# Kernel optimization log

Measured on AMD Instinct MI355X. Metric: run time of the kernel, lower is better.

The kernel has to match this reference:

```python
import math
import jax, jax.numpy as jnp
import numpy as np

NUM_HEADS = 16


def setup_inputs() -> dict:
    key = jax.random.key(0)
    ks = jax.random.split(key, 5)
    B, S, H = 2, 2048, 1024
    hidden_states = jax.random.normal(ks[0], (B, S, H), dtype=jnp.float32)
    # causal lower-triangular float mask [1, 1, S, S], as the module expects
    ltor_mask = jnp.tril(jnp.ones((S, S), dtype=jnp.float32))[None, None, :, :]
    # weights stored pre-transposed: y = x @ W + b (equivalent to torch Linear)
    W_qkv = jax.random.normal(ks[1], (H, 3 * H), dtype=jnp.float32) * (1.0 / math.sqrt(H))
    b_qkv = jnp.zeros((3 * H,), dtype=jnp.float32)
    W_dense = jax.random.normal(ks[2], (H, H), dtype=jnp.float32) * (1.0 / math.sqrt(H))
    b_dense = jnp.zeros((H,), dtype=jnp.float32)
    return {
        "hidden_states": hidden_states,
        "ltor_mask": ltor_mask,
        "W_qkv": W_qkv,
        "b_qkv": b_qkv,
        "W_dense": W_dense,
        "b_dense": b_dense,
    }


def reference(hidden_states, ltor_mask, W_qkv, b_qkv, W_dense, b_dense):
    B, S, H = hidden_states.shape
    nh = NUM_HEADS
    hd = H // nh

    # fused QKV projection: [B, S, 3H] -> split -> [B, nh, S, hd]
    qkv = hidden_states @ W_qkv + b_qkv
    q, k, v = jnp.split(qkv, 3, axis=-1)

    def to_heads(x):
        return x.reshape(B, S, nh, hd).transpose(0, 2, 1, 3)

    q, k, v = to_heads(q), to_heads(k), to_heads(v)

    # scaled dot-product scores [B, nh, S, S]
    scores = jnp.einsum("bhqd,bhkd->bhqk", q, k) / math.sqrt(hd)
    # mul/sub causal masking, exactly as the torch module does
    scores = scores * ltor_mask - 10000.0 * (1.0 - ltor_mask)
    probs = jax.nn.softmax(scores, axis=-1)
    # attention dropout omitted (eval mode / p=0.0)

    ctx = jnp.einsum("bhqk,bhkd->bhqd", probs, v)
    ctx = ctx.transpose(0, 2, 1, 3).reshape(B, S, H)

    out = ctx @ W_dense + b_dense
    # output dropout omitted (eval mode / p=0.0)
    return out
```

## Files before the change

### kernel.cpp

```cpp
#include <hip/hip_runtime.h>
#include <math.h>

#define BATCH 2
#define SEQ   2048
#define HID   1024
#define NHEAD 16
#define HDIM  64
#define MTOT  (BATCH * SEQ)
#define QKVN  (3 * HID)
#define HBUF  ((size_t)BATCH * NHEAD * SEQ * HDIM)

typedef _Float16 f16x8 __attribute__((ext_vector_type(8)));
typedef _Float16 f16x4 __attribute__((ext_vector_type(4)));
typedef float    f32x4 __attribute__((ext_vector_type(4)));

#define MFMA16(a, b, c) __builtin_amdgcn_mfma_f32_16x16x32_f16((a), (b), (c), 0, 0, 0)

#define GLDS16(gp, lp) __builtin_amdgcn_global_load_lds( \
    (const __attribute__((address_space(1))) void*)(gp), \
    (__attribute__((address_space(3))) void*)(lp), 16, 0, 0)

#if __has_builtin(__builtin_amdgcn_exp2f)
#define EXP2F(x) __builtin_amdgcn_exp2f(x)
#else
#define EXP2F(x) exp2f(x)
#endif

#define SCALE2 0.18033688011f
#define MASK2  -14426.950408f
#define BIAS2  -4.0f

__global__ __launch_bounds__(256) void prep_kernel(
    const float* __restrict__ hs, const float* __restrict__ Wqkv,
    const float* __restrict__ Wd, _Float16* __restrict__ A_h,
    _Float16* __restrict__ outQ, _Float16* __restrict__ outD)
{
    __shared__ _Float16 T[32][36];
    const int gid = blockIdx.x;
    const int tid = threadIdx.x;
    if (gid < 2048) {
        const int ci = gid * 256 + tid;
        const int m = ci >> 7, cc = ci & 127;
        const float* src = hs + (size_t)m * 1024 + cc * 8;
        f16x8 o;
#pragma unroll
        for (int j = 0; j < 8; ++j) o[j] = (_Float16)src[j];
        *(f16x8*)(A_h + (size_t)m * 1024 + ((cc >> 3) << 6)
                  + (((cc & 7) ^ (m & 7)) << 3)) = o;
        return;
    }
    const int tb = gid - 2048;
    const int bx = tb & 127, k0 = (tb >> 7) * 32;
    const float* in;
    _Float16* out;
    int N, n0;
    bool isQ;
    if (bx < 96) { in = Wqkv; out = outQ; N = QKVN; n0 = bx * 32; isQ = true; }
    else         { in = Wd;   out = outD; N = HID;  n0 = (bx - 96) * 32; isQ = false; }
    {
        const int r = tid >> 3, c4 = (tid & 7) * 4;
        float4 v = *(const float4*)(in + (size_t)(k0 + r) * N + n0 + c4);
        T[r][c4 + 0] = (_Float16)v.x;
        T[r][c4 + 1] = (_Float16)v.y;
        T[r][c4 + 2] = (_Float16)v.z;
        T[r][c4 + 3] = (_Float16)v.w;
    }
    __syncthreads();
    {
        const int nn = tid >> 3, k4 = (tid & 7) * 4;
        const int n = n0 + nn;
        f16x4 o;
        o[0] = T[k4 + 0][nn]; o[1] = T[k4 + 1][nn];
        o[2] = T[k4 + 2][nn]; o[3] = T[k4 + 3][nn];
        if (isQ) {
            const int cin = (((k0 >> 5) & 1) << 2) | (k4 >> 3);
            const int pos = cin ^ (n & 7);
            *(f16x4*)(out + (size_t)n * 1024 + (k0 & ~63) + pos * 8 + (k4 & 7)) = o;
        } else {
            const int pos = ((k4 >> 3) ^ (n & 3)), half = (k4 >> 2) & 1;
            *(f16x4*)(out + (size_t)n * 1024 + k0 + pos * 8 + half * 4) = o;
        }
    }
}

__global__ __launch_bounds__(512, 2) void qkv_gemm8(
    const _Float16* __restrict__ A, const _Float16* __restrict__ Bt,
    const float* __restrict__ bias, _Float16* __restrict__ base)
{
    __shared__ _Float16 S[2][2][16384];
    const int tid = threadIdx.x;
    const int w = tid >> 6, l = tid & 63;
    const int a = l & 15, q4 = l >> 4, a7 = a & 7;
    const int xc = blockIdx.x & 7, loc = blockIdx.x >> 3;
    const int bx = (xc & 1) * 6 + loc % 6;
    const int by = (xc >> 1) * 4 + loc / 6;
    const int m0 = by * 256, n0 = bx * 256;
    const int wm = (w >> 2) * 128, wn = (w & 3) * 64;

    const int srow = tid >> 3;
    const int scol = (tid & 7) * 8;
    const _Float16* gAs = A  + (size_t)(m0 + srow) * 1024 + scol;
    const _Float16* gBs = Bt + (size_t)(n0 + srow) * 1024 + scol;

    auto stage_u = [&](int u, int kt, int sl) {
        const size_t ko = (size_t)kt * 64;
        if (u < 4)
            GLDS16(gAs + (size_t)u * 65536 + ko, &S[sl][0][0] + u * 4096 + tid * 8);
        else
            GLDS16(gBs + (size_t)(u - 4) * 65536 + ko, &S[sl][1][0] + (u - 4) * 4096 + tid * 8);
    };

#pragma unroll
    for (int u = 0; u < 8; ++u) stage_u(u, 0, 0);
#pragma unroll
    for (int u = 0; u < 8; ++u) stage_u(u, 1, 1);
    asm volatile("s_waitcnt vmcnt(8)" ::: "memory");
    __builtin_amdgcn_sched_barrier(0);
    __builtin_amdgcn_s_barrier();
    __builtin_amdgcn_sched_barrier(0);

    f32x4 acc[8][4];
#pragma unroll
    for (int i = 0; i < 8; ++i)
#pragma unroll
        for (int j = 0; j < 4; ++j) acc[i][j] = (f32x4){0.f, 0.f, 0.f, 0.f};

#define FRG(SP, row_, ks_) \
    (*(const f16x8*)&(SP)[(row_) * 64 + ((((ks_) * 4 + q4) ^ a7) << 3)])

    f16x8 afL[4][2], afH[4][2], bfL[2][2], bfH[2][2];
    {
        const _Float16* sA = &S[0][0][0];
        const _Float16* sB = &S[0][1][0];
#pragma unroll
        for (int i = 0; i < 4; ++i) {
            afL[i][0] = FRG(sA, wm + i * 16 + a, 0);
            afL[i][1] = FRG(sA, wm + i * 16 + a, 1);
        }
#pragma unroll
        for (int j = 0; j < 2; ++j) {
            bfL[j][0] = FRG(sB, wn + j * 16 + a, 0);
            bfL[j][1] = FRG(sB, wn + j * 16 + a, 1);
        }
    }

    for (int t = 0; t < 16; ++t) {
        const int sl = t & 1, nsl = sl ^ 1;
        const _Float16* sA = &S[sl][0][0];
        const _Float16* sB = &S[sl][1][0];
        const bool st = (t >= 1) & (t < 15);

        if (st) {
#pragma unroll
            for (int u = 0; u < 8; ++u) stage_u(u, t + 1, nsl);
        }

        __builtin_amdgcn_s_setprio(1);
#pragma unroll
        for (int i = 0; i < 4; ++i)
#pragma unroll
            for (int j = 0; j < 2; ++j) {
                acc[i][j] = MFMA16(afL[i][0], bfL[j][0], acc[i][j]);
                acc[i][j] = MFMA16(afL[i][1], bfL[j][1], acc[i][j]);
            }
        __builtin_amdgcn_s_setprio(0);

#pragma unroll
        for (int j = 0; j < 2; ++j) {
            bfH[j][0] = FRG(sB, wn + 32 + j * 16 + a, 0);
            bfH[j][1] = FRG(sB, wn + 32 + j * 16 + a, 1);
        }
        __builtin_amdgcn_s_setprio(1);
#pragma unroll
        for (int i = 0; i < 4; ++i)
#pragma unroll
            for (int j = 0; j < 2; ++j) {
                acc[i][j + 2] = MFMA16(afL[i][0], bfH[j][0], acc[i][j + 2]);
                acc[i][j + 2] = MFMA16(afL[i][1], bfH[j][1], acc[i][j + 2]);
            }
        __builtin_amdgcn_s_setprio(0);

#pragma unroll
        for (int i = 0; i < 4; ++i) {
            afH[i][0] = FRG(sA, wm + 64 + i * 16 + a, 0);
            afH[i][1] = FRG(sA, wm + 64 + i * 16 + a, 1);
        }
        __builtin_amdgcn_s_setprio(1);
#pragma unroll
        for (int i = 0; i < 4; ++i)
#pragma unroll
            for (int j = 0; j < 2; ++j) {
                acc[i + 4][j + 2] = MFMA16(afH[i][0], bfH[j][0], acc[i + 4][j + 2]);
                acc[i + 4][j + 2] = MFMA16(afH[i][1], bfH[j][1], acc[i + 4][j + 2]);
            }
#pragma unroll
        for (int i = 0; i < 4; ++i)
#pragma unroll
            for (int j = 0; j < 2; ++j) {
                acc[i + 4][j] = MFMA16(afH[i][0], bfL[j][0], acc[i + 4][j]);
                acc[i + 4][j] = MFMA16(afH[i][1], bfL[j][1], acc[i + 4][j]);
            }
        __builtin_amdgcn_s_setprio(0);

        asm volatile("s_waitcnt vmcnt(0)" ::: "memory");
        __builtin_amdgcn_sched_barrier(0);
        __builtin_amdgcn_s_barrier();
        __builtin_amdgcn_sched_barrier(0);

        if (t < 15) {
            const _Float16* nA = &S[nsl][0][0];
            const _Float16* nB = &S[nsl][1][0];
#pragma unroll
            for (int i = 0; i < 4; ++i) {
                afL[i][0] = FRG(nA, wm + i * 16 + a, 0);
                afL[i][1] = FRG(nA, wm + i * 16 + a, 1);
            }
#pragma unroll
            for (int j = 0; j < 2; ++j) {
                bfL[j][0] = FRG(nB, wn + j * 16 + a, 0);
                bfL[j][1] = FRG(nB, wn + j * 16 + a, 1);
            }
        }
    }
#undef FRG

#pragma unroll
    for (int j = 0; j < 4; ++j) {
        const int n = n0 + wn + 16 * j + a;
        const float bv = bias[n];
        const int tq = n >> 10, h = (n >> 6) & 15, d = n & 63;
#pragma unroll
        for (int i = 0; i < 8; ++i) {
            const int mb = m0 + wm + 16 * i + q4 * 4;
            const int bb = mb >> 11, sb = mb & 2047;
            if (tq == 2) {
                f16x4 ov;
#pragma unroll
                for (int r = 0; r < 4; ++r) ov[r] = (_Float16)(acc[i][j][r] + bv);
                const size_t off =
                    ((size_t)((bb * 16 + h) * 64 + d)) * 2048
                    + (sb & ~63)
                    + ((((sb >> 3) & 7) ^ (d & 7)) << 3) + (sb & 7);
                *(f16x4*)(base + 3 * HBUF + off) = ov;
            } else if (tq == 1) {
#pragma unroll
                for (int r = 0; r < 4; ++r) {
                    const int s = sb + r;
                    const _Float16 val = (_Float16)(acc[i][j][r] + bv);
                    const int dk = ((((d >> 3) ^ (s & 7)) & 7) << 3) | (d & 7);
                    base[HBUF + ((size_t)(bb * 16 + h) * 2048 + s) * 64 + dk] = val;
                }
            } else {
#pragma unroll
                for (int r = 0; r < 4; ++r) {
                    const _Float16 val = (_Float16)(acc[i][j][r] + bv);
                    base[((size_t)(bb * 16 + h) * 2048 + sb + r) * 64 + d] = val;
                }
            }
        }
    }
}

template<int EPI, int TM>
__global__ __launch_bounds__(256) void mfma_gemm(
    const _Float16* __restrict__ A, const _Float16* __restrict__ Bt,
    const float* __restrict__ bias, void* __restrict__ Cout,
    int M, int N, int K)
{
    __shared__ _Float16 As[TM * 32];
    __shared__ _Float16 Bs[128 * 32];
    constexpr int TI = TM / 32;
    constexpr int AR = TM / 4;

    const int tid = threadIdx.x;
    const int w = tid >> 6, l = tid & 63;
    const int a = l & 15, q4 = l >> 4;
    const int m0 = blockIdx.y * TM, n0 = blockIdx.x * 128;
    const int wm = (w >> 1) * (TM / 2), wn = (w & 1) * 64;

    f32x4 acc[TI][4];
#pragma unroll
    for (int i = 0; i < TI; ++i)
#pragma unroll
        for (int j = 0; j < 4; ++j) acc[i][j] = (f32x4){0.f, 0.f, 0.f, 0.f};

    const _Float16* gA = A + (size_t)(m0 + w * AR + (l >> 2)) * K + (l & 3) * 8;
    const _Float16* gB = Bt + (size_t)(n0 + w * 32 + (l >> 2)) * K + (l & 3) * 8;
    _Float16* sA = As + w * AR * 32;
    _Float16* sB = Bs + w * 1024;

    for (int k0 = 0; k0 < K; k0 += 32) {
#pragma unroll
        for (int u = 0; u < TM / 64; ++u)
            GLDS16(gA + (size_t)u * 16 * K + k0, sA + u * 512);
        GLDS16(gB + k0,          sB);
        GLDS16(gB + 16 * K + k0, sB + 512);
        __syncthreads();

        f16x8 af[TI], bf[4];
        const int pa = (q4 ^ (a & 3)) << 3;
#pragma unroll
        for (int i = 0; i < TI; ++i)
            af[i] = *(const f16x8*)&As[(wm + 16 * i + a) * 32 + pa];
#pragma unroll
        for (int j = 0; j < 4; ++j)
            bf[j] = *(const f16x8*)&Bs[(wn + 16 * j + a) * 32 + pa];
#pragma unroll
        for (int i = 0; i < TI; ++i)
#pragma unroll
            for (int j = 0; j < 4; ++j)
                acc[i][j] = MFMA16(af[i], bf[j], acc[i][j]);
        __syncthreads();
    }

    {
        float* C = (float*)Cout;
#pragma unroll
        for (int j = 0; j < 4; ++j) {
            const int n = n0 + wn + 16 * j + a;
            const float bv = bias[n];
#pragma unroll
            for (int i = 0; i < TI; ++i)
#pragma unroll
                for (int r = 0; r < 4; ++r) {
                    const int m = m0 + wm + 16 * i + q4 * 4 + r;
                    C[(size_t)m * N + n] = acc[i][j][r] + bv;
                }
        }
    }
}

__global__ __launch_bounds__(256, 2) void attn_mfma(
    const _Float16* __restrict__ qb, const _Float16* __restrict__ kb,
    const _Float16* __restrict__ vtb, _Float16* __restrict__ ctx)
{
    __shared__ _Float16 Ks[2][64 * 64];
    __shared__ _Float16 VT[2][64 * 64];
    __shared__ _Float16 Ps[4][16 * 64];

    const int bid = blockIdx.x;
    const int jj = bid >> 3;
    const int bhIdx = (bid & 7) * 4 + (jj >> 4);
    const int p = jj & 15;
    const int b = bhIdx >> 4, h = bhIdx & 15;
    const int tid = threadIdx.x;
    const int w = tid >> 6, l = tid & 63;
    const int a = l & 15, q4 = l >> 4, a7 = a & 7;
    const size_t bh  = ((size_t)b * NHEAD + h) * SEQ;
    const size_t bhd = ((size_t)b * NHEAD + h) * 64;

    const int qHi = (31 - p) * 64 + w * 16;
    const int qLo = p * 64 + w * 16;
    const int ntiles = 32 - p;

    f16x8 qfh[2], qfl[2];
    {
        const _Float16* qp = qb + (bh + qHi + a) * 64;
        qfh[0] = *(const f16x8*)(qp + q4 * 8);
        qfh[1] = *(const f16x8*)(qp + 32 + q4 * 8);
        const _Float16* ql = qb + (bh + qLo + a) * 64;
        qfl[0] = *(const f16x8*)(ql + q4 * 8);
        qfl[1] = *(const f16x8*)(ql + 32 + q4 * 8);
    }

    f32x4 Oh[4], Ol[4];
#pragma unroll
    for (int c = 0; c < 4; ++c) {
        Oh[c] = (f32x4){0.f, 0.f, 0.f, 0.f};
        Ol[c] = (f32x4){0.f, 0.f, 0.f, 0.f};
    }
    float lh = 0.f, ll = 0.f;

    const _Float16* kg = kb + (bh + w * 16) * 64 + l * 8;
    const int vrow = w * 16 + (l >> 3);
    const _Float16* vg = vtb + (bhd + vrow) * 2048 + (l & 7) * 8;
    _Float16* pbuf = &Ps[w][0];
    const int p0 = (q4 ^ a7) << 3;

    auto stage = [&](int t, int buf) {
        _Float16* ksl = &Ks[buf][0] + w * 1024 + l * 8;
        const _Float16* kt = kg + (size_t)t * 4096;
        GLDS16(kt,       ksl);
        GLDS16(kt + 512, ksl + 512);
        _Float16* vtl = &VT[buf][0] + vrow * 64 + (l & 7) * 8;
        GLDS16(vg + t * 64,            vtl);
        GLDS16(vg + t * 64 + 8 * 2048, vtl + 512);
    };

    stage(0, 0);

    for (int t = 0; t < ntiles; ++t) {
        __syncthreads();
        if (t + 1 < ntiles) stage(t + 1, (t + 1) & 1);

        const _Float16* ksb  = &Ks[t & 1][0];
        const _Float16* vbuf = &VT[t & 1][0];
        const int kt0 = t * 64;
        const bool doLo = (t <= p);

        f32x4 sh[4], sl[4];
#pragma unroll
        for (int n0 = 0; n0 < 4; ++n0) {
            f16x8 kf0 = *(const f16x8*)&ksb[(n0 * 16 + a) * 64 + p0];
            f16x8 kf1 = *(const f16x8*)&ksb[(n0 * 16 + a) * 64 + (p0 ^ 32)];
            f32x4 c = (f32x4){0.f, 0.f, 0.f, 0.f};
            c = MFMA16(kf0, qfh[0], c);
            c = MFMA16(kf1, qfh[1], c);
            sh[n0] = c;
            if (doLo) {
                f32x4 d = (f32x4){0.f, 0.f, 0.f, 0.f};
                d = MFMA16(kf0, qfl[0], d);
                d = MFMA16(kf1, qfl[1], d);
                sl[n0] = d;
            }
        }

        auto half_step = [&](f32x4 st[4], float& lrun, f32x4* O,
                             const bool maskT, const int qbase) {
            if (maskT) {
#pragma unroll
                for (int n0 = 0; n0 < 4; ++n0)
#pragma unroll
                    for (int r = 0; r < 4; ++r) {
                        const int kgl = kt0 + n0 * 16 + q4 * 4 + r;
                        st[n0][r] = (kgl > qbase + a) ? MASK2
                                                      : fmaf(st[n0][r], SCALE2, BIAS2);
                    }
            } else {
#pragma unroll
                for (int n0 = 0; n0 < 4; ++n0)
#pragma unroll
                    for (int r = 0; r < 4; ++r)
                        st[n0][r] = fmaf(st[n0][r], SCALE2, BIAS2);
            }
            float ls = 0.f;
#pragma unroll
            for (int n0 = 0; n0 < 4; ++n0)
#pragma unroll
                for (int r = 0; r < 4; ++r) {
                    const float pe = EXP2F(st[n0][r]);
                    st[n0][r] = pe;
                    ls += pe;
                }
            lrun += ls;
#pragma unroll
            for (int n0 = 0; n0 < 4; ++n0) {
                f16x4 pk;
#pragma unroll
                for (int r = 0; r < 4; ++r) pk[r] = (_Float16)st[n0][r];
                const int pos = (2 * n0 + (q4 >> 1)) ^ a7;
                *(f16x4*)&pbuf[a * 64 + pos * 8 + ((q4 & 1) << 2)] = pk;
            }
            f16x8 pf0 = *(const f16x8*)&pbuf[a * 64 + p0];
            f16x8 pf1 = *(const f16x8*)&pbuf[a * 64 + (p0 ^ 32)];
#pragma unroll
            for (int c = 0; c < 4; ++c) {
                f16x8 vf0 = *(const f16x8*)&vbuf[(c * 16 + a) * 64 + p0];
                f16x8 vf1 = *(const f16x8*)&vbuf[(c * 16 + a) * 64 + (p0 ^ 32)];
                O[c] = MFMA16(vf0, pf0, O[c]);
                O[c] = MFMA16(vf1, pf1, O[c]);
            }
        };

        half_step(sh, lh, Oh, t == 31 - p, qHi);
        if (doLo) half_step(sl, ll, Ol, t == p, qLo);
    }

    auto finish = [&](float lrun, const f32x4* O, const int qbase) {
        float lt = lrun;
        lt += __shfl_xor(lt, 16);
        lt += __shfl_xor(lt, 32);
        const float inv = 1.0f / lt;
        const size_t row = (size_t)b * SEQ + qbase + a;
#pragma unroll
        for (int c = 0; c < 4; ++c) {
            const int d0 = c * 16 + q4 * 4;
            const int kcol = h * 64 + (d0 & ~31)
                           + ((((d0 >> 3) & 3) ^ (a & 3)) << 3) + (d0 & 7);
            f16x4 ov;
#pragma unroll
            for (int r = 0; r < 4; ++r) ov[r] = (_Float16)(O[c][r] * inv);
            *(f16x4*)(ctx + row * HID + kcol) = ov;
        }
    };
    finish(lh, Oh, qHi);
    finish(ll, Ol, qLo);
}

extern "C" void kernel_launch(void* const* d_in, const int* in_sizes, int n_in,
                              void* d_out, int out_size, void* d_ws, size_t ws_size,
                              hipStream_t stream) {
    const float* hs   = (const float*)d_in[0];
    const float* Wqkv = (const float*)d_in[2];
    const float* bqkv = (const float*)d_in[3];
    const float* Wd   = (const float*)d_in[4];
    const float* bd   = (const float*)d_in[5];

    _Float16* A_h   = (_Float16*)d_ws;
    _Float16* WqkvT = A_h + (size_t)MTOT * HID;
    _Float16* WdT   = WqkvT + (size_t)QKVN * HID;
    _Float16* qbuf  = WdT + (size_t)HID * HID;
    _Float16* ctxb  = qbuf + 4 * HBUF;

    prep_kernel<<<6144, 256, 0, stream>>>(hs, Wqkv, Wd, A_h, WqkvT, WdT);

    qkv_gemm8<<<192, 512, 0, stream>>>(A_h, WqkvT, bqkv, qbuf);

    attn_mfma<<<512, 256, 0, stream>>>(
        qbuf, qbuf + HBUF, qbuf + 3 * HBUF, ctxb);

    mfma_gemm<1, 64><<<dim3(HID / 128, MTOT / 64), 256, 0, stream>>>(
        ctxb, WdT, bd, d_out, MTOT, HID, HID);
}
```

Before: 186.0 us.

## Retile QKV GEMM to 256x192 tiles over 256 blocks, swizzle on load

The QKV projection GEMM switches from 256x256 tiles on 192 blocks to 256x192 tiles on 256 blocks, so the grid matches the 256 compute units of MI355X. The LDS XOR swizzle now happens in the global-address computation at load time rather than in the prep kernel's output layout. The end-of-iteration barrier is skipped on the last tile. The attention kernel also gains s_setprio around its MFMA blocks. The trade-off is lower per-block reuse (an N tile of 192) and one block per CU under the new launch bounds.

Measured after the change: 185.4 us. Within noise of the previous version (-0.3%).

```diff
diff --git a/kernel.cpp b/kernel.cpp
--- a/kernel.cpp
+++ b/kernel.cpp
@@ -45,8 +45,7 @@
         f16x8 o;
 #pragma unroll
         for (int j = 0; j < 8; ++j) o[j] = (_Float16)src[j];
-        *(f16x8*)(A_h + (size_t)m * 1024 + ((cc >> 3) << 6)
-                  + (((cc & 7) ^ (m & 7)) << 3)) = o;
+        *(f16x8*)(A_h + (size_t)m * 1024 + cc * 8) = o;
         return;
     }
     const int tb = gid - 2048;
@@ -73,9 +72,7 @@
         o[0] = T[k4 + 0][nn]; o[1] = T[k4 + 1][nn];
         o[2] = T[k4 + 2][nn]; o[3] = T[k4 + 3][nn];
         if (isQ) {
-            const int cin = (((k0 >> 5) & 1) << 2) | (k4 >> 3);
-            const int pos = cin ^ (n & 7);
-            *(f16x4*)(out + (size_t)n * 1024 + (k0 & ~63) + pos * 8 + (k4 & 7)) = o;
+            *(f16x4*)(out + (size_t)n * 1024 + k0 + k4) = o;
         } else {
             const int pos = ((k4 >> 3) ^ (n & 3)), half = (k4 >> 2) & 1;
             *(f16x4*)(out + (size_t)n * 1024 + k0 + pos * 8 + half * 4) = o;
@@ -83,149 +80,129 @@
     }
 }
 
-__global__ __launch_bounds__(512, 2) void qkv_gemm8(
+__global__ __launch_bounds__(512, 1) void qkv_gemm8(
     const _Float16* __restrict__ A, const _Float16* __restrict__ Bt,
     const float* __restrict__ bias, _Float16* __restrict__ base)
 {
-    __shared__ _Float16 S[2][2][16384];
+    __shared__ _Float16 SA[2][16384];
+    __shared__ _Float16 SB[2][12288];
     const int tid = threadIdx.x;
     const int w = tid >> 6, l = tid & 63;
     const int a = l & 15, q4 = l >> 4, a7 = a & 7;
     const int xc = blockIdx.x & 7, loc = blockIdx.x >> 3;
-    const int bx = (xc & 1) * 6 + loc % 6;
-    const int by = (xc >> 1) * 4 + loc / 6;
-    const int m0 = by * 256, n0 = bx * 256;
-    const int wm = (w >> 2) * 128, wn = (w & 3) * 64;
-
-    const int srow = tid >> 3;
-    const int scol = (tid & 7) * 8;
-    const _Float16* gAs = A  + (size_t)(m0 + srow) * 1024 + scol;
-    const _Float16* gBs = Bt + (size_t)(n0 + srow) * 1024 + scol;
-
-    auto stage_u = [&](int u, int kt, int sl) {
+    const int bx = (xc & 3) * 4 + (loc & 3);
+    const int by = (xc >> 2) * 8 + (loc >> 2);
+    const int m0 = by * 256, n0 = bx * 192;
+    const int wm = (w >> 2) * 128, wn = (w & 3) * 48;
+
+    const int csw = (((tid & 7) ^ ((tid >> 3) & 7)) << 3);
+    const _Float16* gA0 = A  + (size_t)(m0 + (tid >> 3)) * 1024 + csw;
+    const _Float16* gB0 = Bt + (size_t)(n0 + (tid >> 3)) * 1024 + csw;
+
+    auto stage = [&](int kt, int sl) {
         const size_t ko = (size_t)kt * 64;
-        if (u < 4)
-            GLDS16(gAs + (size_t)u * 65536 + ko, &S[sl][0][0] + u * 4096 + tid * 8);
-        else
-            GLDS16(gBs + (size_t)(u - 4) * 65536 + ko, &S[sl][1][0] + (u - 4) * 4096 + tid * 8);
+#pragma unroll
+        for (int u = 0; u < 4; ++u)
+            GLDS16(gA0 + (size_t)(u * 64) * 1024 + ko, &SA[sl][0] + u * 4096 + tid * 8);
+#pragma unroll
+        for (int u = 0; u < 3; ++u)
+            GLDS16(gB0 + (size_t)(u * 64) * 1024 + ko, &SB[sl][0] + u * 4096 + tid * 8);
     };
 
-#pragma unroll
-    for (int u = 0; u < 8; ++u) stage_u(u, 0, 0);
-#pragma unroll
-    for (int u = 0; u < 8; ++u) stage_u(u, 1, 1);
-    asm volatile("s_waitcnt vmcnt(8)" ::: "memory");
+    stage(0, 0); stage(1, 1);
+    asm volatile("s_waitcnt vmcnt(7)" ::: "memory");
     __builtin_amdgcn_sched_barrier(0);
     __builtin_amdgcn_s_barrier();
     __builtin_amdgcn_sched_barrier(0);
 
-    f32x4 acc[8][4];
+    f32x4 acc[8][3];
 #pragma unroll
     for (int i = 0; i < 8; ++i)
 #pragma unroll
-        for (int j = 0; j < 4; ++j) acc[i][j] = (f32x4){0.f, 0.f, 0.f, 0.f};
+        for (int j = 0; j < 3; ++j) acc[i][j] = (f32x4){0.f, 0.f, 0.f, 0.f};
 
 #define FRG(SP, row_, ks_) \
     (*(const f16x8*)&(SP)[(row_) * 64 + ((((ks_) * 4 + q4) ^ a7) << 3)])
 
-    f16x8 afL[4][2], afH[4][2], bfL[2][2], bfH[2][2];
+    f16x8 aL[4][2], aH[4][2], bf[3][2];
     {
-        const _Float16* sA = &S[0][0][0];
-        const _Float16* sB = &S[0][1][0];
 #pragma unroll
         for (int i = 0; i < 4; ++i) {
-            afL[i][0] = FRG(sA, wm + i * 16 + a, 0);
-            afL[i][1] = FRG(sA, wm + i * 16 + a, 1);
+            aL[i][0] = FRG(SA[0], wm + i * 16 + a, 0);
+            aL[i][1] = FRG(SA[0], wm + i * 16 + a, 1);
         }
 #pragma unroll
         for (int j = 0; j < 2; ++j) {
-            bfL[j][0] = FRG(sB, wn + j * 16 + a, 0);
-            bfL[j][1] = FRG(sB, wn + j * 16 + a, 1);
+            bf[j][0] = FRG(SB[0], wn + j * 16 + a, 0);
+            bf[j][1] = FRG(SB[0], wn + j * 16 + a, 1);
         }
     }
 
     for (int t = 0; t < 16; ++t) {
         const int sl = t & 1, nsl = sl ^ 1;
-        const _Float16* sA = &S[sl][0][0];
-        const _Float16* sB = &S[sl][1][0];
-        const bool st = (t >= 1) & (t < 15);
-
-        if (st) {
-#pragma unroll
-            for (int u = 0; u < 8; ++u) stage_u(u, t + 1, nsl);
-        }
+        const _Float16* sA = &SA[sl][0];
+        const _Float16* sB = &SB[sl][0];
+
+        if (t >= 1 && t <= 14) stage(t + 1, nsl);
 
         __builtin_amdgcn_s_setprio(1);
 #pragma unroll
         for (int i = 0; i < 4; ++i)
 #pragma unroll
             for (int j = 0; j < 2; ++j) {
-                acc[i][j] = MFMA16(afL[i][0], bfL[j][0], acc[i][j]);
-                acc[i][j] = MFMA16(afL[i][1], bfL[j][1], acc[i][j]);
+                acc[i][j] = MFMA16(aL[i][0], bf[j][0], acc[i][j]);
+                acc[i][j] = MFMA16(aL[i][1], bf[j][1], acc[i][j]);
             }
         __builtin_amdgcn_s_setprio(0);
 
-#pragma unroll
-        for (int j = 0; j < 2; ++j) {
-            bfH[j][0] = FRG(sB, wn + 32 + j * 16 + a, 0);
-            bfH[j][1] = FRG(sB, wn + 32 + j * 16 + a, 1);
-        }
+        bf[2][0] = FRG(sB, wn + 32 + a, 0);
+        bf[2][1] = FRG(sB, wn + 32 + a, 1);
         __builtin_amdgcn_s_setprio(1);
 #pragma unroll
+        for (int i = 0; i < 4; ++i) {
+            acc[i][2] = MFMA16(aL[i][0], bf[2][0], acc[i][2]);
+            acc[i][2] = MFMA16(aL[i][1], bf[2][1], acc[i][2]);
+        }
+        __builtin_amdgcn_s_setprio(0);
+
+#pragma unroll
+        for (int i = 0; i < 4; ++i) {
+            aH[i][0] = FRG(sA, wm + 64 + i * 16 + a, 0);
+            aH[i][1] = FRG(sA, wm + 64 + i * 16 + a, 1);
+        }
+        __builtin_amdgcn_s_setprio(1);
+#pragma unroll
         for (int i = 0; i < 4; ++i)
 #pragma unroll
+            for (int j = 0; j < 3; ++j) {
+                acc[i + 4][j] = MFMA16(aH[i][0], bf[j][0], acc[i + 4][j]);
+                acc[i + 4][j] = MFMA16(aH[i][1], bf[j][1], acc[i + 4][j]);
+            }
+        __builtin_amdgcn_s_setprio(0);
+
+        if (t < 15) {
+            asm volatile("s_waitcnt vmcnt(0)" ::: "memory");
+            __builtin_amdgcn_sched_barrier(0);
+            __builtin_amdgcn_s_barrier();
+            __builtin_amdgcn_sched_barrier(0);
+            const _Float16* nA = &SA[nsl][0];
+            const _Float16* nB = &SB[nsl][0];
+#pragma unroll
+            for (int i = 0; i < 4; ++i) {
+                aL[i][0] = FRG(nA, wm + i * 16 + a, 0);
+                aL[i][1] = FRG(nA, wm + i * 16 + a, 1);
+            }
+#pragma unroll
             for (int j = 0; j < 2; ++j) {
-                acc[i][j + 2] = MFMA16(afL[i][0], bfH[j][0], acc[i][j + 2]);
-                acc[i][j + 2] = MFMA16(afL[i][1], bfH[j][1], acc[i][j + 2]);
-            }
-        __builtin_amdgcn_s_setprio(0);
-
-#pragma unroll
-        for (int i = 0; i < 4; ++i) {
-            afH[i][0] = FRG(sA, wm + 64 + i * 16 + a, 0);
-            afH[i][1] = FRG(sA, wm + 64 + i * 16 + a, 1);
-        }
-        __builtin_amdgcn_s_setprio(1);
-#pragma unroll
-        for (int i = 0; i < 4; ++i)
-#pragma unroll
-            for (int j = 0; j < 2; ++j) {
-                acc[i + 4][j + 2] = MFMA16(afH[i][0], bfH[j][0], acc[i + 4][j + 2]);
-                acc[i + 4][j + 2] = MFMA16(afH[i][1], bfH[j][1], acc[i + 4][j + 2]);
-            }
-#pragma unroll
-        for (int i = 0; i < 4; ++i)
-#pragma unroll
-            for (int j = 0; j < 2; ++j) {
-                acc[i + 4][j] = MFMA16(afH[i][0], bfL[j][0], acc[i + 4][j]);
-                acc[i + 4][j] = MFMA16(afH[i][1], bfL[j][1], acc[i + 4][j]);
-            }
-        __builtin_amdgcn_s_setprio(0);
-
-        asm volatile("s_waitcnt vmcnt(0)" ::: "memory");
-        __builtin_amdgcn_sched_barrier(0);
-        __builtin_amdgcn_s_barrier();
-        __builtin_amdgcn_sched_barrier(0);
-
-        if (t < 15) {
-            const _Float16* nA = &S[nsl][0][0];
-            const _Float16* nB = &S[nsl][1][0];
-#pragma unroll
-            for (int i = 0; i < 4; ++i) {
-                afL[i][0] = FRG(nA, wm + i * 16 + a, 0);
-                afL[i][1] = FRG(nA, wm + i * 16 + a, 1);
-            }
-#pragma unroll
-            for (int j = 0; j < 2; ++j) {
-                bfL[j][0] = FRG(nB, wn + j * 16 + a, 0);
-                bfL[j][1] = FRG(nB, wn + j * 16 + a, 1);
+                bf[j][0] = FRG(nB, wn + j * 16 + a, 0);
+                bf[j][1] = FRG(nB, wn + j * 16 + a, 1);
             }
         }
     }
 #undef FRG
 
 #pragma unroll
-    for (int j = 0; j < 4; ++j) {
+    for (int j = 0; j < 3; ++j) {
         const int n = n0 + wn + 16 * j + a;
         const float bv = bias[n];
         const int tq = n >> 10, h = (n >> 6) & 15, d = n & 63;
@@ -399,6 +376,7 @@
         const bool doLo = (t <= p);
 
         f32x4 sh[4], sl[4];
+        __builtin_amdgcn_s_setprio(1);
 #pragma unroll
         for (int n0 = 0; n0 < 4; ++n0) {
             f16x8 kf0 = *(const f16x8*)&ksb[(n0 * 16 + a) * 64 + p0];
@@ -414,6 +392,7 @@
                 sl[n0] = d;
             }
         }
+        __builtin_amdgcn_s_setprio(0);
 
         auto half_step = [&](f32x4 st[4], float& lrun, f32x4* O,
                              const bool maskT, const int qbase) {
@@ -453,6 +432,7 @@
             }
             f16x8 pf0 = *(const f16x8*)&pbuf[a * 64 + p0];
             f16x8 pf1 = *(const f16x8*)&pbuf[a * 64 + (p0 ^ 32)];
+            __builtin_amdgcn_s_setprio(1);
 #pragma unroll
             for (int c = 0; c < 4; ++c) {
                 f16x8 vf0 = *(const f16x8*)&vbuf[(c * 16 + a) * 64 + p0];
@@ -460,6 +440,7 @@
                 O[c] = MFMA16(vf0, pf0, O[c]);
                 O[c] = MFMA16(vf1, pf1, O[c]);
             }
+            __builtin_amdgcn_s_setprio(0);
         };
 
         half_step(sh, lh, Oh, t == 31 - p, qHi);
@@ -504,7 +485,7 @@
 
     prep_kernel<<<6144, 256, 0, stream>>>(hs, Wqkv, Wd, A_h, WqkvT, WdT);
 
-    qkv_gemm8<<<192, 512, 0, stream>>>(A_h, WqkvT, bqkv, qbuf);
+    qkv_gemm8<<<256, 512, 0, stream>>>(A_h, WqkvT, bqkv, qbuf);
 
     attn_mfma<<<512, 256, 0, stream>>>(
         qbuf, qbuf + HBUF, qbuf + 3 * HBUF, ctxb);
```
